# Kernel tuning notes

Measured on AMD Instinct MI355X. Metric: run time of the kernel, lower is better.

The kernel has to match this reference:

```python
import jax, jax.numpy as jnp
import numpy as np

N = 20000      # total nodes (100 graphs x 200 nodes)
B = 100        # batch_size
PER = 200      # nodes per graph (uniform) -> max_num_nodes
E = 320000     # edges (before self-loops)
F_IN = 32      # num_features
HEADS = 10
OUT = 128      # output_dim
NEG_SLOPE = 0.2  # PyG GATConv default


def setup_inputs() -> dict:
    key = jax.random.key(0)
    ks = jax.random.split(key, 14)
    feats = jax.random.normal(ks[0], (N, F_IN), jnp.float32)
    src = jax.random.randint(ks[1], (E,), 0, N)
    dst = jax.random.randint(ks[2], (E,), 0, N)
    edge_index = jnp.stack([src, dst]).astype(jnp.int32)
    graph_id = jnp.repeat(jnp.arange(B, dtype=jnp.int32), PER)
    batch_num_nodes = jnp.full((B,), PER, jnp.int32)
    s1 = 1.0 / np.sqrt(F_IN)
    s2 = 1.0 / np.sqrt(F_IN * HEADS)
    s3 = 1.0 / np.sqrt(OUT)
    return {
        "feats": feats,
        "edge_index": edge_index,
        "graph_id": graph_id,
        "batch_num_nodes": batch_num_nodes,
        # GATConv 1: in F_IN -> HEADS x F_IN, concat
        "W1": jax.random.normal(ks[3], (F_IN, HEADS * F_IN), jnp.float32) * s1,
        "a1_src": jax.random.normal(ks[4], (HEADS, F_IN), jnp.float32) * s1,
        "a1_dst": jax.random.normal(ks[5], (HEADS, F_IN), jnp.float32) * s1,
        "b1": jnp.zeros((HEADS * F_IN,), jnp.float32),
        "W2": jax.random.normal(ks[6], (HEADS * F_IN, OUT), jnp.float32) * s2,
        "a2_src": jax.random.normal(ks[7], (1, OUT), jnp.float32) * s3,
        "a2_dst": jax.random.normal(ks[8], (1, OUT), jnp.float32) * s3,
        "b2": jnp.zeros((OUT,), jnp.float32),
        # shared fc_g1
        "fc_w": jax.random.normal(ks[9], (OUT, OUT), jnp.float32) * s3,
        "fc_b": jnp.zeros((OUT,), jnp.float32),
    }


def gat_conv(x, src, dst, W, a_src, a_dst, bias, heads, out_dim):
    # x: [N, Fin]; src/dst already include self-loops (PyG default add_self_loops=True)
    n = x.shape[0]
    xw = (x @ W).reshape(n, heads, out_dim)                 # [N,H,F]
    s_src = jnp.einsum('nhf,hf->nh', xw, a_src)             # [N,H]
    s_dst = jnp.einsum('nhf,hf->nh', xw, a_dst)
    e = jax.nn.leaky_relu(s_src[src] + s_dst[dst], NEG_SLOPE)  # [E,H]
    # segment softmax over incoming edges of each destination node
    m = jax.ops.segment_max(e, dst, num_segments=n)         # [N,H]
    ex = jnp.exp(e - m[dst])
    denom = jax.ops.segment_sum(ex, dst, num_segments=n)    # [N,H]
    alpha = ex / jnp.maximum(denom[dst], 1e-16)             # [E,H]
    out = jax.ops.segment_sum(alpha[:, :, None] * xw[src], dst, num_segments=n)  # [N,H,F]
    return out.reshape(n, heads * out_dim) + bias


def reference(feats, edge_index, graph_id, batch_num_nodes,
              W1, a1_src, a1_dst, b1, W2, a2_src, a2_dst, b2, fc_w, fc_b):
    n = feats.shape[0]
    loops = jnp.arange(n, dtype=edge_index.dtype)
    src = jnp.concatenate([edge_index[0], loops])
    dst = jnp.concatenate([edge_index[1], loops])
    x = feats.astype(jnp.float32)
    # dropout layers are identity in eval mode
    x = jax.nn.elu(gat_conv(x, src, dst, W1, a1_src, a1_dst, b1, HEADS, F_IN))
    x = gat_conv(x, src, dst, W2, a2_src, a2_dst, b2, 1, OUT)
    x = jax.nn.relu(x)                                       # [N, OUT]
    # dgl_split: scatter node feats into [B, max_num_nodes, OUT] padded tensor
    cum = jnp.concatenate([jnp.zeros((1,), jnp.int32),
                           jnp.cumsum(batch_num_nodes).astype(jnp.int32)])
    idx = jnp.arange(n, dtype=jnp.int32) - cum[graph_id] + graph_id * PER
    padded = jnp.zeros((B * PER, OUT), x.dtype).at[idx].set(x).reshape(B, PER, OUT)
    out = jax.nn.relu(padded @ fc_w + fc_b)                  # [B, PER, OUT]
    # global max pool per graph, then shared fc_g1 + relu
    pooled = jax.ops.segment_max(x, graph_id, num_segments=B)  # [B, OUT]
    pooled = jax.nn.relu(pooled @ fc_w + fc_b)
    return (out, pooled)
```

## Files before the change

### kernel.cpp

```cpp
#include <hip/hip_runtime.h>

#define N_NODES 20000
#define N_EDGES 320000
#define ETOT    (N_EDGES + N_NODES)
#define HEADS   10
#define F_IN    32
#define C1      (HEADS * F_IN)
#define C2      128
#define NB      100
#define PER     200
#define CAP     96
#define SSTRIDE 12
#define HSTRIDE 328
#define X2STRIDE 136

typedef __attribute__((ext_vector_type(8))) short bf16x8;
typedef __attribute__((ext_vector_type(4))) float floatx4;
typedef _Float16 f16;
typedef _Float16 f16x2 __attribute__((ext_vector_type(2)));
typedef _Float16 f16x4 __attribute__((ext_vector_type(4)));
typedef _Float16 f16x8 __attribute__((ext_vector_type(8)));

static __device__ __forceinline__ unsigned short f2bf(float f) {
    unsigned int u = __float_as_uint(f);
    unsigned int r = (u + 0x7fffu + ((u >> 16) & 1u)) >> 16;
    return (unsigned short)r;
}

#define SCAT_BLOCKS  ((ETOT + 255) / 256)
#define SCORE_BLOCKS ((N_NODES + 63) / 64)
#define W2P_BLOCKS   ((C1 * C2 + 255) / 256)
#define W1P_BLOCKS   ((HEADS * F_IN * F_IN + 255) / 256)
#define FCP_BLOCKS   ((C2 * C2 + 255) / 256)
#define F16_BLOCKS   ((N_NODES * F_IN / 4 + 255) / 256)
__global__ __launch_bounds__(256) void mega_prep_kernel(
        const int* __restrict__ ei, int* __restrict__ cursor, int* __restrict__ csr_src,
        const float* __restrict__ feats, f16* __restrict__ feats16,
        const float* __restrict__ W1, unsigned short* __restrict__ W1p,
        const float* __restrict__ W2, unsigned short* __restrict__ W2p,
        const float* __restrict__ fcw, f16* __restrict__ FCp,
        const float* __restrict__ a1s, const float* __restrict__ a1d,
        float* __restrict__ s_src, float* __restrict__ s_dst) {
    unsigned int b = blockIdx.x;
    if (b < SCAT_BLOCKS) {
        int e = b * 256 + threadIdx.x;
        if (e >= ETOT) return;
        int s, d;
        if (e < N_EDGES) { s = ei[e]; d = ei[N_EDGES + e]; }
        else             { s = e - N_EDGES; d = s; }
        int pos = atomicAdd(&cursor[d], 1);
        csr_src[(size_t)d * CAP + pos] = s;
        return;
    }
    b -= SCAT_BLOCKS;
    if (b < SCORE_BLOCKS) {
        __shared__ __align__(16) float A[64 * F_IN];
        __shared__ float Ws[C1], Wd[C1];
        int t = threadIdx.x;
        for (int o = t; o < C1; o += 256) {
            int k = o & 31, h = o >> 5;
            float ss = 0.f, dd = 0.f;
#pragma unroll
            for (int f = 0; f < F_IN; f++) {
                float wv = W1[k * C1 + h * 32 + f];
                ss += wv * a1s[h * 32 + f];
                dd += wv * a1d[h * 32 + f];
            }
            Ws[k * HEADS + h] = ss;
            Wd[k * HEADS + h] = dd;
        }
        int n0 = b * 64;
        int nrows = min(64, N_NODES - n0);
        const float4* fs = (const float4*)(feats + (size_t)n0 * F_IN);
        float4* Af = (float4*)A;
        for (int i = t; i < nrows * 8; i += 256) Af[i] = fs[i];
        __syncthreads();
        for (int o = t; o < nrows * HEADS; o += 256) {
            int nl = o / HEADS, h = o - nl * HEADS;
            const float* ar = A + nl * F_IN;
            float ss = 0.f, dd = 0.f;
#pragma unroll
            for (int k = 0; k < F_IN; k++) {
                float av = ar[k];
                ss += av * Ws[k * HEADS + h];
                dd += av * Wd[k * HEADS + h];
            }
            s_src[(size_t)(n0 + nl) * SSTRIDE + h] = ss;
            s_dst[(size_t)(n0 + nl) * SSTRIDE + h] = dd;
        }
        return;
    }
    b -= SCORE_BLOCKS;
    if (b < W2P_BLOCKS) {
        int o = b * 256 + threadIdx.x;
        if (o >= C1 * C2) return;
        int j    = o & 7;
        int lane = (o >> 3) & 63;
        int ct   = (o >> 9) & 7;
        int kb   = o >> 12;
        int k = kb * 32 + (lane >> 4) * 8 + j;
        int n = ct * 16 + (lane & 15);
        W2p[o] = f2bf(W2[k * C2 + n]);
        return;
    }
    b -= W2P_BLOCKS;
    if (b < W1P_BLOCKS) {
        int o = b * 256 + threadIdx.x;
        if (o >= HEADS * F_IN * F_IN) return;
        int j    = o & 7;
        int lane = (o >> 3) & 63;
        int ct   = (o >> 9) & 1;
        int h    = o >> 10;
        int k = (lane >> 4) * 8 + j;
        int f = ct * 16 + (lane & 15);
        W1p[o] = f2bf(W1[k * C1 + h * 32 + f]);
        return;
    }
    b -= W1P_BLOCKS;
    if (b < FCP_BLOCKS) {
        int o = b * 256 + threadIdx.x;
        if (o >= C2 * C2) return;
        int j    = o & 7;
        int lane = (o >> 3) & 63;
        int ct   = (o >> 9) & 7;
        int kb   = o >> 12;
        int k = kb * 32 + (lane >> 4) * 8 + j;
        int n = ct * 16 + (lane & 15);
        FCp[o] = (f16)fcw[k * C2 + n];
        return;
    }
    b -= FCP_BLOCKS;
    {
        int o = b * 256 + threadIdx.x;
        if (o < N_NODES * F_IN / 4) {
            float4 v = ((const float4*)feats)[o];
            f16* d = feats16 + 4 * o;
            d[0] = (f16)v.x; d[1] = (f16)v.y; d[2] = (f16)v.z; d[3] = (f16)v.w;
        }
    }
}

__global__ __launch_bounds__(512) void agg1h1g2_kernel(
        const f16* __restrict__ feats16, const float* __restrict__ s_src,
        const float* __restrict__ s_dst, const int* __restrict__ deg_arr,
        const int* __restrict__ csr_src,
        const unsigned short* __restrict__ W1p, const float* __restrict__ b1,
        const unsigned short* __restrict__ W2p,
        const float* __restrict__ a_src, const float* __restrict__ a_dst,
        f16* __restrict__ xw2h, float* __restrict__ s_src2, float* __restrict__ s_dst2) {
    union Smem {
        struct { f16 P[16][HEADS * 32]; int S[16][32]; } p1;
        unsigned short H[16 * HSTRIDE];
    };
    __shared__ __align__(16) Smem u;
    __shared__ __align__(16) unsigned short G[16 * HSTRIDE];
    __shared__ float redS[8][16], redD[8][16];

    int tid   = threadIdx.x;
    int wslot = tid >> 6;
    int lane  = tid & 63;
    int r     = tid >> 5;
    int l     = tid & 31;
    int row0  = blockIdx.x * 16;
    f16* P = u.p1.P[r];
    int* S = u.p1.S[r];
    const f16x2 ones = {(f16)1.f, (f16)1.f};
    const char* fb = (const char*)feats16 + 2 * l;

    {
        int n = row0 + r;
        int beg = n * CAP, deg = deg_arr[n];
        const float* sdp = s_dst + (size_t)n * SSTRIDE;
        float sd[10];
        {
            float4 v0 = *(const float4*)(sdp);
            float4 v1 = *(const float4*)(sdp + 4);
            float2 v2 = *(const float2*)(sdp + 8);
            sd[0]=v0.x; sd[1]=v0.y; sd[2]=v0.z; sd[3]=v0.w;
            sd[4]=v1.x; sd[5]=v1.y; sd[6]=v1.z; sd[7]=v1.w;
            sd[8]=v2.x; sd[9]=v2.y;
        }
        float g[10], la[10];
#pragma unroll
        for (int h = 0; h < 10; h++) { g[h] = 0.f; la[h] = 0.f; }

        for (int c0 = 0; c0 < deg; c0 += 32) {
            int dc = min(deg - c0, 32);
            bool act = l < dc;
            int s_e = csr_src[beg + c0 + min(l, dc - 1)];
            const float* ssp = s_src + (size_t)s_e * SSTRIDE;
            float ss[10];
            {
                float4 v0 = *(const float4*)(ssp);
                float4 v1 = *(const float4*)(ssp + 4);
                float2 v2 = *(const float2*)(ssp + 8);
                ss[0]=v0.x; ss[1]=v0.y; ss[2]=v0.z; ss[3]=v0.w;
                ss[4]=v1.x; ss[5]=v1.y; ss[6]=v1.z; ss[7]=v1.w;
                ss[8]=v2.x; ss[9]=v2.y;
            }
            float p[10];
#pragma unroll
            for (int h = 0; h < 10; h++) {
                float e0 = ss[h] + sd[h];
                e0 = (e0 >= 0.f) ? e0 : 0.2f * e0;
                p[h] = act ? __expf(e0) : 0.f;
            }
            S[l] = s_e << 6;
#pragma unroll
            for (int h = 0; h < 10; h++) P[h * 32 + l] = (f16)p[h];
            asm volatile("s_waitcnt lgkmcnt(0)" ::: "memory");

            int dcp = (dc + 3) & ~3;
            for (int i = 0; i < dcp; i += 4) {
                int4 ss4 = *(const int4*)&S[i];
                f16x2 v01, v23;
                v01.x = *(const f16*)(fb + ss4.x);
                v01.y = *(const f16*)(fb + ss4.y);
                v23.x = *(const f16*)(fb + ss4.z);
                v23.y = *(const f16*)(fb + ss4.w);
#pragma unroll
                for (int h = 0; h < 10; h++) {
                    f16x4 pp = *(const f16x4*)&P[h * 32 + i];
                    f16x2 p01 = {pp[0], pp[1]};
                    f16x2 p23 = {pp[2], pp[3]};
                    g[h]  = __builtin_amdgcn_fdot2(p01, v01, g[h], false);
                    g[h]  = __builtin_amdgcn_fdot2(p23, v23, g[h], false);
                    la[h] = __builtin_amdgcn_fdot2(p01, ones, la[h], false);
                    la[h] = __builtin_amdgcn_fdot2(p23, ones, la[h], false);
                }
            }
            asm volatile("s_waitcnt lgkmcnt(0)" ::: "memory");
        }
        unsigned short* gr = &G[r * HSTRIDE + l];
#pragma unroll
        for (int h = 0; h < 10; h++)
            gr[h * 32] = f2bf(g[h] / fmaxf(la[h], 1e-16f));
    }
    __syncthreads();

    int quad = lane >> 4, col = lane & 15;
    for (int h = wslot; h < 10; h += 8) {
        bf16x8 a = *(const bf16x8*)&G[col * HSTRIDE + h * 32 + quad * 8];
        bf16x8 bA = ((const bf16x8*)W1p)[(h * 2 + 0) * 64 + lane];
        bf16x8 bB = ((const bf16x8*)W1p)[(h * 2 + 1) * 64 + lane];
        floatx4 z = {0.f, 0.f, 0.f, 0.f};
        floatx4 c0 = __builtin_amdgcn_mfma_f32_16x16x32_bf16(a, bA, z, 0, 0, 0);
        floatx4 c1 = __builtin_amdgcn_mfma_f32_16x16x32_bf16(a, bB, z, 0, 0, 0);
        float bias0 = b1[h * 32 + col];
        float bias1 = b1[h * 32 + 16 + col];
#pragma unroll
        for (int reg = 0; reg < 4; reg++) {
            int rr = quad * 4 + reg;
            float o0 = c0[reg] + bias0;
            float o1 = c1[reg] + bias1;
            o0 = (o0 > 0.f) ? o0 : (__expf(o0) - 1.f);
            o1 = (o1 > 0.f) ? o1 : (__expf(o1) - 1.f);
            u.H[rr * HSTRIDE + h * 32 + col]      = f2bf(o0);
            u.H[rr * HSTRIDE + h * 32 + 16 + col] = f2bf(o1);
        }
    }
    __syncthreads();

    floatx4 acc = {0.f, 0.f, 0.f, 0.f};
    const bf16x8* pb = (const bf16x8*)W2p;
#pragma unroll
    for (int kb = 0; kb < 10; kb++) {
        bf16x8 a = *(const bf16x8*)&u.H[col * HSTRIDE + kb * 32 + quad * 8];
        bf16x8 b = pb[(kb * 8 + wslot) * 64 + lane];
        acc = __builtin_amdgcn_mfma_f32_16x16x32_bf16(a, b, acc, 0, 0, 0);
    }
    float asv = a_src[wslot * 16 + col];
    float adv = a_dst[wslot * 16 + col];
#pragma unroll
    for (int reg = 0; reg < 4; reg++) {
        int row = row0 + quad * 4 + reg;
        float v = acc[reg];
        xw2h[(size_t)row * C2 + wslot * 16 + col] = (f16)v;
        float vs = v * asv, vd = v * adv;
#pragma unroll
        for (int off = 8; off >= 1; off >>= 1) {
            vs += __shfl_xor(vs, off);
            vd += __shfl_xor(vd, off);
        }
        if (col == 0) { redS[wslot][quad * 4 + reg] = vs; redD[wslot][quad * 4 + reg] = vd; }
    }
    __syncthreads();
    if (wslot == 0) {
        if (lane < 16) {
            float s = 0.f;
#pragma unroll
            for (int w2 = 0; w2 < 8; w2++) s += redS[w2][lane];
            s_src2[row0 + lane] = s;
        } else if (lane < 32) {
            int r2 = lane - 16;
            float d = 0.f;
#pragma unroll
            for (int w2 = 0; w2 < 8; w2++) d += redD[w2][r2];
            s_dst2[row0 + r2] = d;
        }
    }
}

template <int PASS>
__global__ __launch_bounds__(512) void agg2pass_kernel(
        const f16* __restrict__ xw2h, const float* __restrict__ s_src2,
        const float* __restrict__ s_dst2, const int* __restrict__ deg_arr,
        const int* __restrict__ csr_src, const float* __restrict__ b2,
        f16* __restrict__ Xh0, const f16* __restrict__ FCp,
        const float* __restrict__ fcb,
        float* __restrict__ out, int* __restrict__ pooledi) {
    __shared__ __align__(16) int2 shE[16][32];
    __shared__ __align__(16) f16 X[16 * X2STRIDE];
    int tid   = threadIdx.x;
    int wslot = tid >> 6;
    int lane  = tid & 63;
    int r     = tid >> 5;
    int l     = tid & 31;
    int row0  = blockIdx.x * 16;
    int2* E = shE[r];
    const char* xb = (const char*)xw2h + PASS * 128 + 4 * l;

    {
        int n = row0 + r;
        int beg = n * CAP, deg = deg_arr[n];
        float sd = s_dst2[n];
        float ldn = 0.f, a0 = 0.f, a1 = 0.f;

        for (int c0 = 0; c0 < deg; c0 += 32) {
            int dc = min(deg - c0, 32);
            bool act = l < dc;
            int s_e = csr_src[beg + c0 + min(l, dc - 1)];
            float e = s_src2[s_e] + sd;
            e = (e >= 0.f) ? e : 0.2f * e;
            float p = act ? __expf(e) : 0.f;
            float su = p;
#pragma unroll
            for (int off = 16; off >= 1; off >>= 1) su += __shfl_xor(su, off);
            ldn += su;

            E[l] = make_int2(s_e << 8, __float_as_int(p));
            asm volatile("s_waitcnt lgkmcnt(0)" ::: "memory");

            int dcr = (dc + 3) & ~3;
            for (int i = 0; i < dcr; i += 4) {
                int4 e01 = *(const int4*)&E[i];
                int4 e23 = *(const int4*)&E[i + 2];
                f16x2 v0 = *(const f16x2*)(xb + e01.x);
                f16x2 v1 = *(const f16x2*)(xb + e01.z);
                f16x2 v2 = *(const f16x2*)(xb + e23.x);
                f16x2 v3 = *(const f16x2*)(xb + e23.z);
                float p0 = __int_as_float(e01.y), p1 = __int_as_float(e01.w);
                float p2 = __int_as_float(e23.y), p3 = __int_as_float(e23.w);
                a0 += p0 * (float)v0.x + p1 * (float)v1.x + p2 * (float)v2.x + p3 * (float)v3.x;
                a1 += p0 * (float)v0.y + p1 * (float)v1.y + p2 * (float)v2.y + p3 * (float)v3.y;
            }
            asm volatile("s_waitcnt lgkmcnt(0)" ::: "memory");
        }

        float linv = 1.f / fmaxf(ldn, 1e-16f);
        float2 bb = *(const float2*)(b2 + PASS * 64 + 2 * l);
        f16x2 o;
        o.x = (f16)fmaxf(a0 * linv + bb.x, 0.f);
        o.y = (f16)fmaxf(a1 * linv + bb.y, 0.f);
        if (PASS == 0) {
            *(f16x2*)&Xh0[(size_t)n * 64 + 2 * l] = o;
        } else {
            *(f16x2*)&X[r * X2STRIDE + 64 + 2 * l] = o;
            *(f16x2*)&X[r * X2STRIDE + 2 * l] =
                *(const f16x2*)&Xh0[(size_t)(row0 + r) * 64 + 2 * l];
        }
    }
    if (PASS == 0) return;
    __syncthreads();

    int quad = lane >> 4, col = lane & 15;
    floatx4 acc = {0.f, 0.f, 0.f, 0.f};
    const f16x8* pb = (const f16x8*)FCp;
#pragma unroll
    for (int kb = 0; kb < 4; kb++) {
        f16x8 a = *(const f16x8*)&X[col * X2STRIDE + kb * 32 + quad * 8];
        f16x8 b = pb[(kb * 8 + wslot) * 64 + lane];
        acc = __builtin_amdgcn_mfma_f32_16x16x32_f16(a, b, acc, 0, 0, 0);
    }
    float bias = fcb[wslot * 16 + col];
#pragma unroll
    for (int reg = 0; reg < 4; reg++) {
        int row = row0 + quad * 4 + reg;
        out[(size_t)row * C2 + wslot * 16 + col] = fmaxf(acc[reg] + bias, 0.f);
    }

    if (tid < C2) {
        int c = tid;
        int gA = row0 / PER;
        int gB = (row0 + 15) / PER;
        float mA = 0.f, mB = 0.f;
#pragma unroll
        for (int rr = 0; rr < 16; rr++) {
            float v = (float)X[rr * X2STRIDE + c];
            if ((row0 + rr) / PER == gA) mA = fmaxf(mA, v);
            else                         mB = fmaxf(mB, v);
        }
        atomicMax(&pooledi[gA * C2 + c], __float_as_int(mA));
        if (gB != gA) atomicMax(&pooledi[gB * C2 + c], __float_as_int(mB));
    }
}

__global__ void poolfc_kernel(const int* __restrict__ pooledi, const float* __restrict__ fcw,
                              const float* __restrict__ fcb, float* __restrict__ outp) {
    __shared__ float mx[C2];
    int g = blockIdx.x, t = threadIdx.x;
    mx[t] = __int_as_float(pooledi[g * C2 + t]);
    __syncthreads();
    float acc = 0.f;
    for (int k = 0; k < C2; k++) acc += mx[k] * fcw[k * C2 + t];
    outp[g * C2 + t] = fmaxf(acc + fcb[t], 0.f);
}

extern "C" void kernel_launch(void* const* d_in, const int* in_sizes, int n_in,
                              void* d_out, int out_size, void* d_ws, size_t ws_size,
                              hipStream_t stream) {
    const float* feats = (const float*)d_in[0];
    const int*   ei    = (const int*)d_in[1];
    const float* W1  = (const float*)d_in[4];
    const float* a1s = (const float*)d_in[5];
    const float* a1d = (const float*)d_in[6];
    const float* b1  = (const float*)d_in[7];
    const float* W2  = (const float*)d_in[8];
    const float* a2s = (const float*)d_in[9];
    const float* a2d = (const float*)d_in[10];
    const float* b2  = (const float*)d_in[11];
    const float* fcw = (const float*)d_in[12];
    const float* fcb = (const float*)d_in[13];

    float* out_main = (float*)d_out;
    float* out_pool = (float*)d_out + (size_t)N_NODES * C2;

    char* p = (char*)d_ws;
    auto alloc = [&](size_t bytes) {
        char* r = p;
        p += (bytes + 255) & ~(size_t)255;
        return r;
    };
    unsigned short* W2p  = (unsigned short*)alloc(sizeof(short) * C1 * C2);
    unsigned short* W1p  = (unsigned short*)alloc(sizeof(short) * HEADS * F_IN * F_IN);
    f16*   FCp     = (f16*)alloc(sizeof(f16) * C2 * C2);
    f16*   feats16 = (f16*)alloc(sizeof(f16) * (size_t)N_NODES * F_IN);
    f16*   xw2h    = (f16*)alloc(sizeof(f16) * (size_t)N_NODES * C2);
    f16*   Xh0     = (f16*)alloc(sizeof(f16) * (size_t)N_NODES * 64);
    float* s1s    = (float*)alloc(sizeof(float) * N_NODES * SSTRIDE);
    float* s1d    = (float*)alloc(sizeof(float) * N_NODES * SSTRIDE);
    float* s2s    = (float*)alloc(sizeof(float) * N_NODES);
    float* s2d    = (float*)alloc(sizeof(float) * N_NODES);
    const int NZ = N_NODES + NB * C2;
    int* zeros   = (int*)alloc(sizeof(int) * NZ);
    int* cursor  = zeros;
    int* pooledi = zeros + N_NODES;
    int* csr_src = (int*)alloc(sizeof(int) * N_NODES * CAP);

    hipMemsetAsync(zeros, 0, sizeof(int) * NZ, stream);

    mega_prep_kernel<<<SCAT_BLOCKS + SCORE_BLOCKS + W2P_BLOCKS + W1P_BLOCKS + FCP_BLOCKS + F16_BLOCKS,
                       256, 0, stream>>>(
        ei, cursor, csr_src, feats, feats16, W1, W1p, W2, W2p, fcw, FCp,
        a1s, a1d, s1s, s1d);

    agg1h1g2_kernel<<<1250, 512, 0, stream>>>(feats16, s1s, s1d, cursor, csr_src,
                                              W1p, b1, W2p, a2s, a2d, xw2h, s2s, s2d);
    agg2pass_kernel<0><<<1250, 512, 0, stream>>>(xw2h, s2s, s2d, cursor, csr_src, b2,
                                                 Xh0, FCp, fcb, out_main, pooledi);
    agg2pass_kernel<1><<<1250, 512, 0, stream>>>(xw2h, s2s, s2d, cursor, csr_src, b2,
                                                 Xh0, FCp, fcb, out_main, pooledi);
    poolfc_kernel<<<NB, C2, 0, stream>>>(pooledi, fcw, fcb, out_pool);
}
```

Baseline: 158.7 us.

## Fuse layer-2 aggregation passes and pool FC, use shuffles with prefetch

Merges the two half-width layer-2 aggregation kernels into one kernel where each lane handles four channels, and drops the Xh0 intermediate buffer. The pooled FC is folded in through a last-block-per-graph counter pattern, which removes the separate poolfc launch. In layer-1 and layer-2 aggregation, shared-memory staging of edge offsets and weights is replaced by wave shuffles, and the next group's gathers are software-prefetched. The costs are more registers per thread, a completion counter of 13 blocks per graph that relies on fences and atomics, and the pool FC running serially inside a few blocks.

```diff
diff --git a/kernel.cpp b/kernel.cpp
--- a/kernel.cpp
+++ b/kernel.cpp
@@ -149,7 +149,7 @@
         const float* __restrict__ a_src, const float* __restrict__ a_dst,
         f16* __restrict__ xw2h, float* __restrict__ s_src2, float* __restrict__ s_dst2) {
     union Smem {
-        struct { f16 P[16][HEADS * 32]; int S[16][32]; } p1;
+        f16 P[16][HEADS * 32];
         unsigned short H[16 * HSTRIDE];
     };
     __shared__ __align__(16) Smem u;
@@ -162,8 +162,7 @@
     int r     = tid >> 5;
     int l     = tid & 31;
     int row0  = blockIdx.x * 16;
-    f16* P = u.p1.P[r];
-    int* S = u.p1.S[r];
+    f16* P = u.P[r];
     const f16x2 ones = {(f16)1.f, (f16)1.f};
     const char* fb = (const char*)feats16 + 2 * l;
 
@@ -205,29 +204,36 @@
                 e0 = (e0 >= 0.f) ? e0 : 0.2f * e0;
                 p[h] = act ? __expf(e0) : 0.f;
             }
-            S[l] = s_e << 6;
+            int s_off = s_e << 6;
 #pragma unroll
             for (int h = 0; h < 10; h++) P[h * 32 + l] = (f16)p[h];
+
+            int o0 = __shfl(s_off, 0, 32), o1 = __shfl(s_off, 1, 32);
+            int o2 = __shfl(s_off, 2, 32), o3 = __shfl(s_off, 3, 32);
+            f16x2 vA01, vA23;
+            vA01.x = *(const f16*)(fb + o0); vA01.y = *(const f16*)(fb + o1);
+            vA23.x = *(const f16*)(fb + o2); vA23.y = *(const f16*)(fb + o3);
             asm volatile("s_waitcnt lgkmcnt(0)" ::: "memory");
 
             int dcp = (dc + 3) & ~3;
             for (int i = 0; i < dcp; i += 4) {
-                int4 ss4 = *(const int4*)&S[i];
-                f16x2 v01, v23;
-                v01.x = *(const f16*)(fb + ss4.x);
-                v01.y = *(const f16*)(fb + ss4.y);
-                v23.x = *(const f16*)(fb + ss4.z);
-                v23.y = *(const f16*)(fb + ss4.w);
+                int j = (i + 4 < dcp) ? i + 4 : i;
+                int n0o = __shfl(s_off, j + 0, 32), n1o = __shfl(s_off, j + 1, 32);
+                int n2o = __shfl(s_off, j + 2, 32), n3o = __shfl(s_off, j + 3, 32);
+                f16x2 vB01, vB23;
+                vB01.x = *(const f16*)(fb + n0o); vB01.y = *(const f16*)(fb + n1o);
+                vB23.x = *(const f16*)(fb + n2o); vB23.y = *(const f16*)(fb + n3o);
 #pragma unroll
                 for (int h = 0; h < 10; h++) {
                     f16x4 pp = *(const f16x4*)&P[h * 32 + i];
                     f16x2 p01 = {pp[0], pp[1]};
                     f16x2 p23 = {pp[2], pp[3]};
-                    g[h]  = __builtin_amdgcn_fdot2(p01, v01, g[h], false);
-                    g[h]  = __builtin_amdgcn_fdot2(p23, v23, g[h], false);
+                    g[h]  = __builtin_amdgcn_fdot2(p01, vA01, g[h], false);
+                    g[h]  = __builtin_amdgcn_fdot2(p23, vA23, g[h], false);
                     la[h] = __builtin_amdgcn_fdot2(p01, ones, la[h], false);
                     la[h] = __builtin_amdgcn_fdot2(p23, ones, la[h], false);
                 }
+                vA01 = vB01; vA23 = vB23;
             }
             asm volatile("s_waitcnt lgkmcnt(0)" ::: "memory");
         }
@@ -301,30 +307,31 @@
     }
 }
 
-template <int PASS>
-__global__ __launch_bounds__(512) void agg2pass_kernel(
+__global__ __launch_bounds__(512) void agg2fc_kernel(
         const f16* __restrict__ xw2h, const float* __restrict__ s_src2,
         const float* __restrict__ s_dst2, const int* __restrict__ deg_arr,
         const int* __restrict__ csr_src, const float* __restrict__ b2,
-        f16* __restrict__ Xh0, const f16* __restrict__ FCp,
-        const float* __restrict__ fcb,
-        float* __restrict__ out, int* __restrict__ pooledi) {
-    __shared__ __align__(16) int2 shE[16][32];
+        const f16* __restrict__ FCp, const float* __restrict__ fcb,
+        const float* __restrict__ fcw,
+        float* __restrict__ out, float* __restrict__ outp,
+        int* __restrict__ pooledi, int* __restrict__ done) {
     __shared__ __align__(16) f16 X[16 * X2STRIDE];
+    __shared__ float pool_mx[C2];
+    __shared__ float pool_part[4][C2];
+    __shared__ int win_s[2];
     int tid   = threadIdx.x;
     int wslot = tid >> 6;
     int lane  = tid & 63;
     int r     = tid >> 5;
     int l     = tid & 31;
     int row0  = blockIdx.x * 16;
-    int2* E = shE[r];
-    const char* xb = (const char*)xw2h + PASS * 128 + 4 * l;
+    const char* xb = (const char*)xw2h + 8 * l;
 
     {
         int n = row0 + r;
         int beg = n * CAP, deg = deg_arr[n];
         float sd = s_dst2[n];
-        float ldn = 0.f, a0 = 0.f, a1 = 0.f;
+        float ldn = 0.f, a0 = 0.f, a1 = 0.f, a2 = 0.f, a3 = 0.f;
 
         for (int c0 = 0; c0 < deg; c0 += 32) {
             int dc = min(deg - c0, 32);
@@ -338,39 +345,44 @@
             for (int off = 16; off >= 1; off >>= 1) su += __shfl_xor(su, off);
             ldn += su;
 
-            E[l] = make_int2(s_e << 8, __float_as_int(p));
-            asm volatile("s_waitcnt lgkmcnt(0)" ::: "memory");
-
+            int s_off = s_e << 8;
             int dcr = (dc + 3) & ~3;
+            float pA0 = __shfl(p, 0, 32), pA1 = __shfl(p, 1, 32);
+            float pA2 = __shfl(p, 2, 32), pA3 = __shfl(p, 3, 32);
+            int oA0 = __shfl(s_off, 0, 32), oA1 = __shfl(s_off, 1, 32);
+            int oA2 = __shfl(s_off, 2, 32), oA3 = __shfl(s_off, 3, 32);
+            f16x4 vA0 = *(const f16x4*)(xb + oA0);
+            f16x4 vA1 = *(const f16x4*)(xb + oA1);
+            f16x4 vA2 = *(const f16x4*)(xb + oA2);
+            f16x4 vA3 = *(const f16x4*)(xb + oA3);
             for (int i = 0; i < dcr; i += 4) {
-                int4 e01 = *(const int4*)&E[i];
-                int4 e23 = *(const int4*)&E[i + 2];
-                f16x2 v0 = *(const f16x2*)(xb + e01.x);
-                f16x2 v1 = *(const f16x2*)(xb + e01.z);
-                f16x2 v2 = *(const f16x2*)(xb + e23.x);
-                f16x2 v3 = *(const f16x2*)(xb + e23.z);
-                float p0 = __int_as_float(e01.y), p1 = __int_as_float(e01.w);
-                float p2 = __int_as_float(e23.y), p3 = __int_as_float(e23.w);
-                a0 += p0 * (float)v0.x + p1 * (float)v1.x + p2 * (float)v2.x + p3 * (float)v3.x;
-                a1 += p0 * (float)v0.y + p1 * (float)v1.y + p2 * (float)v2.y + p3 * (float)v3.y;
+                int j = (i + 4 < dcr) ? i + 4 : i;
+                float pB0 = __shfl(p, j + 0, 32), pB1 = __shfl(p, j + 1, 32);
+                float pB2 = __shfl(p, j + 2, 32), pB3 = __shfl(p, j + 3, 32);
+                int oB0 = __shfl(s_off, j + 0, 32), oB1 = __shfl(s_off, j + 1, 32);
+                int oB2 = __shfl(s_off, j + 2, 32), oB3 = __shfl(s_off, j + 3, 32);
+                f16x4 vB0 = *(const f16x4*)(xb + oB0);
+                f16x4 vB1 = *(const f16x4*)(xb + oB1);
+                f16x4 vB2 = *(const f16x4*)(xb + oB2);
+                f16x4 vB3 = *(const f16x4*)(xb + oB3);
+                a0 += pA0 * (float)vA0[0] + pA1 * (float)vA1[0] + pA2 * (float)vA2[0] + pA3 * (float)vA3[0];
+                a1 += pA0 * (float)vA0[1] + pA1 * (float)vA1[1] + pA2 * (float)vA2[1] + pA3 * (float)vA3[1];
+                a2 += pA0 * (float)vA0[2] + pA1 * (float)vA1[2] + pA2 * (float)vA2[2] + pA3 * (float)vA3[2];
+                a3 += pA0 * (float)vA0[3] + pA1 * (float)vA1[3] + pA2 * (float)vA2[3] + pA3 * (float)vA3[3];
+                pA0 = pB0; pA1 = pB1; pA2 = pB2; pA3 = pB3;
+                vA0 = vB0; vA1 = vB1; vA2 = vB2; vA3 = vB3;
             }
-            asm volatile("s_waitcnt lgkmcnt(0)" ::: "memory");
         }
 
         float linv = 1.f / fmaxf(ldn, 1e-16f);
-        float2 bb = *(const float2*)(b2 + PASS * 64 + 2 * l);
-        f16x2 o;
-        o.x = (f16)fmaxf(a0 * linv + bb.x, 0.f);
-        o.y = (f16)fmaxf(a1 * linv + bb.y, 0.f);
-        if (PASS == 0) {
-            *(f16x2*)&Xh0[(size_t)n * 64 + 2 * l] = o;
-        } else {
-            *(f16x2*)&X[r * X2STRIDE + 64 + 2 * l] = o;
-            *(f16x2*)&X[r * X2STRIDE + 2 * l] =
-                *(const f16x2*)&Xh0[(size_t)(row0 + r) * 64 + 2 * l];
-        }
-    }
-    if (PASS == 0) return;
+        float4 bb = *(const float4*)(b2 + 4 * l);
+        f16x4 o;
+        o[0] = (f16)fmaxf(a0 * linv + bb.x, 0.f);
+        o[1] = (f16)fmaxf(a1 * linv + bb.y, 0.f);
+        o[2] = (f16)fmaxf(a2 * linv + bb.z, 0.f);
+        o[3] = (f16)fmaxf(a3 * linv + bb.w, 0.f);
+        *(f16x4*)&X[r * X2STRIDE + 4 * l] = o;
+    }
     __syncthreads();
 
     int quad = lane >> 4, col = lane & 15;
@@ -389,10 +401,10 @@
         out[(size_t)row * C2 + wslot * 16 + col] = fmaxf(acc[reg] + bias, 0.f);
     }
 
+    int gA = row0 / PER;
+    int gB = (row0 + 15) / PER;
     if (tid < C2) {
         int c = tid;
-        int gA = row0 / PER;
-        int gB = (row0 + 15) / PER;
         float mA = 0.f, mB = 0.f;
 #pragma unroll
         for (int rr = 0; rr < 16; rr++) {
@@ -403,17 +415,36 @@
         atomicMax(&pooledi[gA * C2 + c], __float_as_int(mA));
         if (gB != gA) atomicMax(&pooledi[gB * C2 + c], __float_as_int(mB));
     }
-}
-
-__global__ void poolfc_kernel(const int* __restrict__ pooledi, const float* __restrict__ fcw,
-                              const float* __restrict__ fcb, float* __restrict__ outp) {
-    __shared__ float mx[C2];
-    int g = blockIdx.x, t = threadIdx.x;
-    mx[t] = __int_as_float(pooledi[g * C2 + t]);
     __syncthreads();
-    float acc = 0.f;
-    for (int k = 0; k < C2; k++) acc += mx[k] * fcw[k * C2 + t];
-    outp[g * C2 + t] = fmaxf(acc + fcb[t], 0.f);
+
+    if (tid == 0) {
+        __threadfence();
+        int tA = atomicAdd(&done[gA], 1);
+        int wA = (tA == 12);
+        int wB = 0;
+        if (gB != gA) { int tB = atomicAdd(&done[gB], 1); wB = (tB == 12); }
+        win_s[0] = wA; win_s[1] = wB;
+    }
+    __syncthreads();
+
+    auto pool_fc = [&](int g2) {
+        int t = tid;
+        if (t < C2)
+            pool_mx[t] = __int_as_float(atomicMax(&pooledi[g2 * C2 + t], 0));
+        __syncthreads();
+        int pc = t & (C2 - 1), piece = t >> 7;
+        float acc2 = 0.f;
+        const float* fw = fcw + (size_t)(piece * 32) * C2 + pc;
+        const float* mp = pool_mx + piece * 32;
+        for (int k = 0; k < 32; k++) acc2 += mp[k] * fw[(size_t)k * C2];
+        pool_part[piece][pc] = acc2;
+        __syncthreads();
+        if (piece == 0)
+            outp[(size_t)g2 * C2 + pc] = fmaxf(pool_part[0][pc] + pool_part[1][pc] +
+                                               pool_part[2][pc] + pool_part[3][pc] + fcb[pc], 0.f);
+    };
+    if (win_s[0]) pool_fc(gA);
+    if (win_s[1]) pool_fc(gB);
 }
 
 extern "C" void kernel_launch(void* const* d_in, const int* in_sizes, int n_in,
@@ -446,15 +477,15 @@
     f16*   FCp     = (f16*)alloc(sizeof(f16) * C2 * C2);
     f16*   feats16 = (f16*)alloc(sizeof(f16) * (size_t)N_NODES * F_IN);
     f16*   xw2h    = (f16*)alloc(sizeof(f16) * (size_t)N_NODES * C2);
-    f16*   Xh0     = (f16*)alloc(sizeof(f16) * (size_t)N_NODES * 64);
     float* s1s    = (float*)alloc(sizeof(float) * N_NODES * SSTRIDE);
     float* s1d    = (float*)alloc(sizeof(float) * N_NODES * SSTRIDE);
     float* s2s    = (float*)alloc(sizeof(float) * N_NODES);
     float* s2d    = (float*)alloc(sizeof(float) * N_NODES);
-    const int NZ = N_NODES + NB * C2;
+    const int NZ = N_NODES + NB * C2 + NB;
     int* zeros   = (int*)alloc(sizeof(int) * NZ);
     int* cursor  = zeros;
     int* pooledi = zeros + N_NODES;
+    int* done    = zeros + N_NODES + NB * C2;
     int* csr_src = (int*)alloc(sizeof(int) * N_NODES * CAP);
 
     hipMemsetAsync(zeros, 0, sizeof(int) * NZ, stream);
@@ -466,9 +497,7 @@
 
     agg1h1g2_kernel<<<1250, 512, 0, stream>>>(feats16, s1s, s1d, cursor, csr_src,
                                               W1p, b1, W2p, a2s, a2d, xw2h, s2s, s2d);
-    agg2pass_kernel<0><<<1250, 512, 0, stream>>>(xw2h, s2s, s2d, cursor, csr_src, b2,
-                                                 Xh0, FCp, fcb, out_main, pooledi);
-    agg2pass_kernel<1><<<1250, 512, 0, stream>>>(xw2h, s2s, s2d, cursor, csr_src, b2,
-                                                 Xh0, FCp, fcb, out_main, pooledi);
-    poolfc_kernel<<<NB, C2, 0, stream>>>(pooledi, fcw, fcb, out_pool);
+    agg2fc_kernel<<<1250, 512, 0, stream>>>(xw2h, s2s, s2d, cursor, csr_src, b2,
+                                            FCp, fcb, fcw, out_main, out_pool,
+                                            pooledi, done);
 }
```

After: 190.6 us. +20.1%, slower.
